# Optimization experiments

Hardware: AMD Instinct MI355X
Metric: run time of the kernel (lower is better)

Reference implementation:

```python
import jax, jax.numpy as jnp
import numpy as np

N_KNN = 16
BN_EPS = 1e-5


def conv1d(x, w, b):
    # x: [B, Cin, N], w: [Cout, Cin], b: [Cout] (1x1 Conv1d)
    return jnp.einsum('oc,bcn->bon', w, x) + b[None, :, None]


def conv2d(x, w, b):
    # x: [B, Cin, N, K], w: [Cout, Cin], b: [Cout] (1x1 Conv2d)
    return jnp.einsum('oc,bcnk->bonk', w, x) + b[None, :, None, None]


def bn2d(x, gamma, beta, mean, var):
    # eval-mode BatchNorm2d over channel axis 1
    scale = (gamma / jnp.sqrt(var + BN_EPS))[None, :, None, None]
    return (x - mean[None, :, None, None]) * scale + beta[None, :, None, None]


def knn_idx(pos, k):
    # pos: [B, 3, N] -> idx: [B, N, K] of k nearest neighbors (incl. self)
    p = jnp.swapaxes(pos, 1, 2)  # [B, N, 3]
    sq = jnp.sum(p * p, axis=-1)  # [B, N]
    d2 = sq[:, :, None] - 2.0 * jnp.einsum('bnd,bmd->bnm', p, p) + sq[:, None, :]
    _, idx = jax.lax.top_k(-d2, k)
    return idx


def group(x, idx):
    # x: [B, C, N], idx: [B, N, K] -> [B, C, N, K] (grouping_operation)
    return jax.vmap(lambda xb, ib: xb[:, ib])(x, idx)


def setup_inputs() -> dict:
    key = jax.random.key(0)
    B, C_OBJ, C_Q, N, DIM, PH, AM = 4, 512, 512, 4096, 128, 64, 4
    ks = jax.random.split(key, 32)
    r = lambda i, sh, s=0.05: jax.random.normal(ks[i], sh, jnp.float32) * s
    inp = {
        'obj_feature': jax.random.normal(ks[0], (B, C_OBJ, N), jnp.float32),
        'pos': jax.random.normal(ks[1], (B, 3, N), jnp.float32),
        'query_points': jax.random.normal(ks[2], (B, C_Q, N), jnp.float32),
        # linear_start_query / linear_start_obj
        'w_sq': r(3, (DIM, C_Q)), 'b_sq': r(4, (DIM,)),
        'w_so': r(5, (DIM, C_OBJ)), 'b_so': r(6, (DIM,)),
        # key / query / value 1x1 convs
        'w_k': r(7, (DIM, DIM)), 'b_k': r(8, (DIM,)),
        'w_q': r(9, (DIM, DIM)), 'b_q': r(10, (DIM,)),
        'w_v': r(11, (DIM, DIM)), 'b_v': r(12, (DIM,)),
        # pos_mlp: Conv2d(3->PH), BN, ReLU, Conv2d(PH->DIM)
        'w_p1': r(13, (PH, 3)), 'b_p1': r(14, (PH,)),
        'g_bn1': 1.0 + r(15, (PH,)), 'be_bn1': r(16, (PH,)),
        'm_bn1': r(17, (PH,)), 'v_bn1': 1.0 + 0.1 * jax.random.uniform(ks[18], (PH,), jnp.float32),
        'w_p2': r(19, (DIM, PH)), 'b_p2': r(20, (DIM,)),
        # attn_mlp: Conv2d(DIM->DIM*AM), BN, ReLU, Conv2d(DIM*AM->DIM)
        'w_a1': r(21, (DIM * AM, DIM)), 'b_a1': r(22, (DIM * AM,)),
        'g_bn2': 1.0 + r(23, (DIM * AM,)), 'be_bn2': r(24, (DIM * AM,)),
        'm_bn2': r(25, (DIM * AM,)), 'v_bn2': 1.0 + 0.1 * jax.random.uniform(ks[26], (DIM * AM,), jnp.float32),
        # linear_end
        'w_e': r(27, (C_OBJ, DIM)), 'b_e': r(28, (C_OBJ,)),
    }
    return inp


def reference(obj_feature, pos, query_points, w_sq, b_sq, w_so, b_so, w_k, b_k,
              w_q, b_q, w_v, b_v, w_p1, b_p1, g_bn1, be_bn1, m_bn1, v_bn1,
              w_p2, b_p2, w_a1, b_a1, g_bn2, be_bn2, m_bn2, v_bn2, w_e, b_e):
    qf = conv1d(query_points, w_sq, b_sq)          # [B, dim, N]
    f = conv1d(obj_feature, w_so, b_so)            # [B, dim, N]
    idx = knn_idx(jax.lax.stop_gradient(pos), N_KNN)  # [B, N, K]
    key_g = group(conv1d(f, w_k, b_k), idx)        # [B, dim, N, K]
    value = conv1d(f, w_v, b_v)                    # [B, dim, N]
    query = conv1d(qf, w_q, b_q)                   # [B, dim, N]
    qk_rel = query[:, :, :, None] - key_g          # [B, dim, N, K]
    pos_rel = pos[:, :, :, None] - group(pos, idx)  # [B, 3, N, K]
    pe = conv2d(jax.nn.relu(bn2d(conv2d(pos_rel, w_p1, b_p1), g_bn1, be_bn1, m_bn1, v_bn1)), w_p2, b_p2)
    attn = conv2d(jax.nn.relu(bn2d(conv2d(qk_rel + pe, w_a1, b_a1), g_bn2, be_bn2, m_bn2, v_bn2)), w_a2_placeholder := w_p2 * 0 + 0, b_p2 * 0) if False else None
    hidden = jax.nn.relu(bn2d(conv2d(qk_rel + pe, w_a1, b_a1), g_bn2, be_bn2, m_bn2, v_bn2))
    attn = jax.nn.softmax(conv2d(hidden, w_a2, b_a2), axis=-1)  # softmax over K
    v = value[:, :, :, None] + pe                  # [B, dim, N, K]
    agg = jnp.sum(attn * v, axis=-1)               # 'b c i j, b c i j -> b c i'
    return conv1d(agg, w_e, b_e)                   # [B, C_obj, N]

# fix: w_a2/b_a2 are parameters; re-declare reference cleanly to include them

def _setup_extra(inp):
    kk = jax.random.split(jax.random.key(7), 2)
    inp['w_a2'] = jax.random.normal(kk[0], (128, 512), jnp.float32) * 0.05
    inp['b_a2'] = jax.random.normal(kk[1], (128,), jnp.float32) * 0.05
    return inp

_orig_setup = setup_inputs

def setup_inputs():
    return _setup_extra(_orig_setup())


def reference(obj_feature, pos, query_points, w_sq, b_sq, w_so, b_so, w_k, b_k,
              w_q, b_q, w_v, b_v, w_p1, b_p1, g_bn1, be_bn1, m_bn1, v_bn1,
              w_p2, b_p2, w_a1, b_a1, g_bn2, be_bn2, m_bn2, v_bn2, w_a2, b_a2,
              w_e, b_e):
    qf = conv1d(query_points, w_sq, b_sq)
    f = conv1d(obj_feature, w_so, b_so)
    idx = knn_idx(jax.lax.stop_gradient(pos), N_KNN)
    key_g = group(conv1d(f, w_k, b_k), idx)
    value = conv1d(f, w_v, b_v)
    query = conv1d(qf, w_q, b_q)
    qk_rel = query[:, :, :, None] - key_g
    pos_rel = pos[:, :, :, None] - group(pos, idx)
    pe = conv2d(jax.nn.relu(bn2d(conv2d(pos_rel, w_p1, b_p1), g_bn1, be_bn1, m_bn1, v_bn1)), w_p2, b_p2)
    hidden = jax.nn.relu(bn2d(conv2d(qk_rel + pe, w_a1, b_a1), g_bn2, be_bn2, m_bn2, v_bn2))
    attn = jax.nn.softmax(conv2d(hidden, w_a2, b_a2), axis=-1)
    v = value[:, :, :, None] + pe
    agg = jnp.sum(attn * v, axis=-1)
    return conv1d(agg, w_e, b_e)
```

## Files before the change

### kernel.cpp

```cpp
#include <hip/hip_runtime.h>

typedef __bf16 bf16;
typedef __bf16 bf16x8 __attribute__((ext_vector_type(8)));
typedef __bf16 bf16x4 __attribute__((ext_vector_type(4)));
typedef __bf16 bf16x2 __attribute__((ext_vector_type(2)));
typedef float f32x4 __attribute__((ext_vector_type(4)));

#define MFMA16(a,b,c) __builtin_amdgcn_mfma_f32_16x16x32_bf16((a),(b),(c),0,0,0)

#define NPTS 4096
#define CIN 512
#define DIM 128
#define PH 64
#define HID 512

#define OFF_WQS 0u
#define OFF_WKO (128u*1024u)
#define OFF_WVO (256u*1024u)
#define OFF_BQS (384u*1024u)
#define OFF_BKO (385u*1024u)
#define OFF_BVO (386u*1024u)
#define OFF_S1  (387u*1024u)
#define OFF_T1  (388u*1024u)
#define OFF_S2  (389u*1024u)
#define OFF_T2  (391u*1024u)
#define OFF_CW  (400u*1024u)
#define OFF_QT  (1u<<20)
#define OFF_KT  (OFF_QT + (4u<<20))
#define OFF_VT  (OFF_QT + (8u<<20))
#define OFF_IDX (OFF_QT + (12u<<20))
#define WS_NEED (OFF_QT + (13u<<20))

struct P {
  const float* in[31];
  char* ws;
  float* out;
};

__global__ __launch_bounds__(256) void k_fold(P p) {
  int tid = blockIdx.x*256 + threadIdx.x;
  char* ws = p.ws;
  if (tid < 196608) {
    int m_id = tid >> 16, o = (tid >> 9) & 127, c = tid & 511;
    const float* A  = m_id==0 ? p.in[9] : (m_id==1 ? p.in[7] : p.in[11]);
    const float* Bm = (m_id==0) ? p.in[3] : p.in[5];
    float acc = 0.f;
    #pragma unroll 8
    for (int m=0;m<128;m++) acc += A[o*128+m] * Bm[m*512+c];
    bf16* outw = (bf16*)(ws + (m_id==0?OFF_WQS: m_id==1?OFF_WKO:OFF_WVO));
    outw[o*512+c] = (bf16)acc;
  } else if (tid < 196992) {
    int t = tid - 196608; int m_id = t >> 7, o = t & 127;
    const float* A  = m_id==0 ? p.in[9] : (m_id==1 ? p.in[7] : p.in[11]);
    const float* bb = (m_id==0) ? p.in[4] : p.in[6];
    const float* bs = m_id==0 ? p.in[10] : (m_id==1 ? p.in[8] : p.in[12]);
    float acc = bs[o];
    for (int m=0;m<128;m++) acc += A[o*128+m] * bb[m];
    float* ob = (float*)(ws + (m_id==0?OFF_BQS: m_id==1?OFF_BKO:OFF_BVO));
    ob[o] = acc;
  } else if (tid < 197056) {
    int i = tid - 196992;
    float s = p.in[15][i] * rsqrtf(p.in[18][i] + 1e-5f);
    ((float*)(ws+OFF_S1))[i] = s;
    ((float*)(ws+OFF_T1))[i] = (p.in[14][i] - p.in[17][i])*s + p.in[16][i];
  } else if (tid < 197568) {
    int i = tid - 197056;
    float s = p.in[23][i] * rsqrtf(p.in[26][i] + 1e-5f);
    ((float*)(ws+OFF_S2))[i] = s;
    ((float*)(ws+OFF_T2))[i] = (p.in[22][i] - p.in[25][i])*s + p.in[24][i];
  } else if (tid < 223168) {
    int e0 = (tid - 197568) * 8;
    const float* src; int base;
    if (e0 < 8192)        { src = p.in[19]; base = 0; }
    else if (e0 < 73728)  { src = p.in[21]; base = 8192; }
    else if (e0 < 139264) { src = p.in[29]; base = 73728; }
    else                  { src = p.in[27]; base = 139264; }
    const float* sp = src + (e0 - base);
    f32x4 a = *(const f32x4*)sp, b2 = *(const f32x4*)(sp+4);
    bf16x8 o8;
    o8[0]=(bf16)a[0]; o8[1]=(bf16)a[1]; o8[2]=(bf16)a[2]; o8[3]=(bf16)a[3];
    o8[4]=(bf16)b2[0]; o8[5]=(bf16)b2[1]; o8[6]=(bf16)b2[2]; o8[7]=(bf16)b2[3];
    *(bf16x8*)((bf16*)(ws+OFF_CW) + e0) = o8;
  }
}

__global__ __launch_bounds__(256) void k_knn(P p) {
  int lane = threadIdx.x & 63, w = threadIdx.x >> 6;
  int ig = blockIdx.x*4 + w;
  int b = ig >> 12, n = ig & 4095;
  const float* pb = p.in[1] + b*3*NPTS;
  float qx = pb[n], qy = pb[NPTS+n], qz = pb[2*NPTS+n];
  float sqn = __fadd_rn(__fadd_rn(__fmul_rn(qx,qx), __fmul_rn(qy,qy)), __fmul_rn(qz,qz));
  float d2a[64];
  #pragma unroll
  for (int t=0;t<64;t++) {
    int j = t*64 + lane;
    float xj=pb[j], yj=pb[NPTS+j], zj=pb[2*NPTS+j];
    float sqj = __fadd_rn(__fadd_rn(__fmul_rn(xj,xj), __fmul_rn(yj,yj)), __fmul_rn(zj,zj));
    float dot = __fadd_rn(__fadd_rn(__fmul_rn(qx,xj), __fmul_rn(qy,yj)), __fmul_rn(qz,zj));
    d2a[t] = __fadd_rn(__fsub_rn(sqn, __fmul_rn(2.f,dot)), sqj);
  }
  int* op = (int*)(p.ws + OFF_IDX) + ig*16;
  long long prev = -1ll;
  for (int r=0;r<16;r++) {
    long long best = 0x7fffffffffffffffll;
    #pragma unroll
    for (int t=0;t<64;t++) {
      long long key = ((long long)(int)__float_as_uint(d2a[t]) << 32) | (long long)(t*64+lane);
      if (key > prev && key < best) best = key;
    }
    #pragma unroll
    for (int off=32; off>0; off>>=1) {
      long long o = __shfl_xor(best, off);
      best = best < o ? best : o;
    }
    prev = best;
    if (lane==0) op[r] = (int)best & 4095;
  }
}

__global__ __launch_bounds__(256) void k_qkv(P p) {
  int mat = blockIdx.z, b = blockIdx.y, n0 = blockIdx.x*64;
  int tid = threadIdx.x, lane = tid&63, w = tid>>6;
  const float* in = (mat==0 ? p.in[2] : p.in[0]) + b*CIN*NPTS;
  const bf16* W = (const bf16*)(p.ws + (mat==0?OFF_WQS: mat==1?OFF_WKO:OFF_WVO));
  const float* bias = (const float*)(p.ws + (mat==0?OFF_BQS: mat==1?OFF_BKO:OFF_BVO));
  bf16* outT = (bf16*)(p.ws + (mat==0?OFF_QT: mat==1?OFF_KT:OFF_VT)) + (b*NPTS + n0)*DIM;
  __shared__ __align__(16) bf16 Bl[64*40];
  f32x4 acc[8] = {};
  for (int ks=0; ks<16; ks++) {
    int c0 = ks*32;
    {
      int cc = tid>>3, nn0 = (tid&7)*8;
      const float* sp = in + (c0+cc)*NPTS + n0 + nn0;
      f32x4 a = *(const f32x4*)sp, b2 = *(const f32x4*)(sp+4);
      Bl[(nn0+0)*40+cc]=(bf16)a[0];  Bl[(nn0+1)*40+cc]=(bf16)a[1];
      Bl[(nn0+2)*40+cc]=(bf16)a[2];  Bl[(nn0+3)*40+cc]=(bf16)a[3];
      Bl[(nn0+4)*40+cc]=(bf16)b2[0]; Bl[(nn0+5)*40+cc]=(bf16)b2[1];
      Bl[(nn0+6)*40+cc]=(bf16)b2[2]; Bl[(nn0+7)*40+cc]=(bf16)b2[3];
    }
    __syncthreads();
    int ncol = w*16 + (lane&15);
    bf16x8 bfr = *(const bf16x8*)(&Bl[ncol*40 + (lane>>4)*8]);
    #pragma unroll
    for (int ot=0;ot<8;ot++) {
      bf16x8 af = *(const bf16x8*)(W + (ot*16 + (lane&15))*CIN + c0 + (lane>>4)*8);
      acc[ot] = MFMA16(af, bfr, acc[ot]);
    }
    __syncthreads();
  }
  int o0 = (lane>>4)*4;
  int nloc = w*16 + (lane&15);
  #pragma unroll
  for (int ot=0;ot<8;ot++) {
    f32x4 bs = *(const f32x4*)(bias + ot*16 + o0);
    bf16x4 st;
    st[0]=(bf16)(acc[ot][0]+bs[0]); st[1]=(bf16)(acc[ot][1]+bs[1]);
    st[2]=(bf16)(acc[ot][2]+bs[2]); st[3]=(bf16)(acc[ot][3]+bs[3]);
    *(bf16x4*)(outT + nloc*DIM + ot*16 + o0) = st;
  }
}

__global__ __launch_bounds__(512) void k_fused(P p) {
  int b = blockIdx.y, pt0 = blockIdx.x*8;
  int tid=threadIdx.x, lane=tid&63, w=tid>>6;
  char* ws = p.ws;
  const bf16* qT = (const bf16*)(ws+OFF_QT) + b*NPTS*DIM;
  const bf16* kT = (const bf16*)(ws+OFF_KT) + b*NPTS*DIM;
  const bf16* vT = (const bf16*)(ws+OFF_VT) + b*NPTS*DIM;
  const int* idxg = (const int*)(ws+OFF_IDX) + (b*NPTS + pt0)*16;
  const bf16* wp2b = (const bf16*)(ws+OFF_CW);
  const bf16* wa1b = wp2b + 8192;
  const bf16* wa2b = wa1b + 65536;
  const bf16* web  = wa2b + 65536;
  __shared__ __align__(16) bf16 Xl[128*136];
  __shared__ __align__(16) bf16 HT[128*72];
  __shared__ __align__(16) bf16 aggl[16*136];
  __shared__ float prl[128][4];
  __shared__ int idxl[128];

  if (tid < 128) {
    int pt = tid>>4;
    int j = idxg[tid] & 4095;
    idxl[tid] = j;
    const float* pb = p.in[1] + b*3*NPTS;
    int n = pt0+pt;
    prl[tid][0] = pb[n]        - pb[j];
    prl[tid][1] = pb[NPTS+n]   - pb[NPTS+j];
    prl[tid][2] = pb[2*NPTS+n] - pb[2*NPTS+j];
  } else if (tid >= 256 && tid < 392) {
    f32x4 z = {};
    *(f32x4*)((char*)aggl + 2176 + (tid-256)*16) = z;
  }
  __syncthreads();

  {
    int col = tid & 127, mb = (tid>>7)*16;
    float r0=prl[col][0], r1=prl[col][1], r2=prl[col][2];
    const float* wp1 = p.in[13];
    const float* s1 = (const float*)(ws+OFF_S1);
    const float* t1 = (const float*)(ws+OFF_T1);
    #pragma unroll
    for (int i=0;i<16;i+=2) {
      int m = mb+i;
      float x0 = wp1[m*3]*r0   + wp1[m*3+1]*r1 + wp1[m*3+2]*r2;
      float x1 = wp1[m*3+3]*r0 + wp1[m*3+4]*r1 + wp1[m*3+5]*r2;
      bf16x2 pk;
      pk[0] = (bf16)fmaxf(0.f, x0*s1[m]   + t1[m]);
      pk[1] = (bf16)fmaxf(0.f, x1*s1[m+1] + t1[m+1]);
      *(bf16x2*)(&HT[col*72 + m]) = pk;
    }
  }
  __syncthreads();

  {
    f32x4 acc[8] = {};
    int crow = w*16 + (lane&15);
    #pragma unroll
    for (int ksx=0; ksx<2; ksx++) {
      int m0 = ksx*32 + (lane>>4)*8;
      bf16x8 af = *(const bf16x8*)(wp2b + crow*PH + m0);
      #pragma unroll
      for (int nt=0; nt<8; nt++) {
        int col = nt*16 + (lane&15);
        bf16x8 bfr = *(const bf16x8*)(&HT[col*72 + m0]);
        acc[nt] = MFMA16(af, bfr, acc[nt]);
      }
    }
    int c0 = w*16 + (lane>>4)*4;
    f32x4 bp4 = *(const f32x4*)(p.in[20] + c0);
    #pragma unroll
    for (int nt=0; nt<8; nt++) {
      int col = nt*16 + (lane&15);
      int j = idxl[col];
      int n = pt0 + nt;
      bf16x4 q4 = *(const bf16x4*)(qT + n*DIM + c0);
      bf16x4 k4 = *(const bf16x4*)(kT + j*DIM + c0);
      bf16x4 st;
      #pragma unroll
      for (int r=0;r<4;r++)
        st[r] = (bf16)((float)q4[r] - (float)k4[r] + acc[nt][r] + bp4[r]);
      *(bf16x4*)(&Xl[col*136 + c0]) = st;
    }
  }
  __syncthreads();

  f32x4 S[8] = {};
  const float* s2 = (const float*)(ws+OFF_S2);
  const float* t2 = (const float*)(ws+OFF_T2);
  for (int ch=0; ch<8; ch++) {
    f32x4 acc1[4] = {};
    int mtw = w & 3, nbase = (w>>2)*4;
    int hrow = ch*64 + mtw*16 + (lane&15);
    #pragma unroll
    for (int ksx=0; ksx<4; ksx++) {
      bf16x8 af = *(const bf16x8*)(wa1b + hrow*DIM + ksx*32 + (lane>>4)*8);
      #pragma unroll
      for (int i=0; i<4; i++) {
        int col = (nbase+i)*16 + (lane&15);
        bf16x8 bfr = *(const bf16x8*)(&Xl[col*136 + ksx*32 + (lane>>4)*8]);
        acc1[i] = MFMA16(af, bfr, acc1[i]);
      }
    }
    int h0 = ch*64 + mtw*16 + (lane>>4)*4;
    int h0loc = mtw*16 + (lane>>4)*4;
    f32x4 sv = *(const f32x4*)(s2 + h0);
    f32x4 tv = *(const f32x4*)(t2 + h0);
    #pragma unroll
    for (int i=0;i<4;i++) {
      int col = (nbase+i)*16 + (lane&15);
      bf16x4 st;
      st[0]=(bf16)fmaxf(0.f, acc1[i][0]*sv[0]+tv[0]);
      st[1]=(bf16)fmaxf(0.f, acc1[i][1]*sv[1]+tv[1]);
      st[2]=(bf16)fmaxf(0.f, acc1[i][2]*sv[2]+tv[2]);
      st[3]=(bf16)fmaxf(0.f, acc1[i][3]*sv[3]+tv[3]);
      *(bf16x4*)(&HT[col*72 + h0loc]) = st;
    }
    __syncthreads();
    int orow = w*16 + (lane&15);
    #pragma unroll
    for (int ksx=0; ksx<2; ksx++) {
      bf16x8 af = *(const bf16x8*)(wa2b + orow*HID + ch*64 + ksx*32 + (lane>>4)*8);
      #pragma unroll
      for (int nt=0; nt<8; nt++) {
        int col = nt*16 + (lane&15);
        bf16x8 bfr = *(const bf16x8*)(&HT[col*72 + ksx*32 + (lane>>4)*8]);
        S[nt] = MFMA16(af, bfr, S[nt]);
      }
    }
    __syncthreads();
  }

  {
    int c0 = w*16 + (lane>>4)*4;
    #pragma unroll
    for (int nt=0; nt<8; nt++) {
      f32x4 s = S[nt];
      float at[4];
      #pragma unroll
      for (int r=0;r<4;r++) {
        float mx = s[r];
        #pragma unroll
        for (int mk=8; mk; mk>>=1) mx = fmaxf(mx, __shfl_xor(mx, mk));
        float e = __expf(s[r]-mx);
        float sum = e;
        #pragma unroll
        for (int mk=8; mk; mk>>=1) sum += __shfl_xor(sum, mk);
        at[r] = e / sum;
      }
      int col = nt*16 + (lane&15);
      int j = idxl[col];
      int n = pt0 + nt;
      bf16x4 x4 = *(const bf16x4*)(&Xl[col*136 + c0]);
      bf16x4 q4 = *(const bf16x4*)(qT + n*DIM + c0);
      bf16x4 k4 = *(const bf16x4*)(kT + j*DIM + c0);
      bf16x4 v4 = *(const bf16x4*)(vT + n*DIM + c0);
      float ag[4];
      #pragma unroll
      for (int r=0;r<4;r++) {
        float vpe = (float)v4[r] + (float)x4[r] - (float)q4[r] + (float)k4[r];
        float cab = at[r]*vpe;
        #pragma unroll
        for (int mk=8; mk; mk>>=1) cab += __shfl_xor(cab, mk);
        ag[r] = cab;
      }
      if ((lane&15)==0) {
        bf16x4 st;
        st[0]=(bf16)ag[0]; st[1]=(bf16)ag[1]; st[2]=(bf16)ag[2]; st[3]=(bf16)ag[3];
        *(bf16x4*)(&aggl[nt*136 + c0]) = st;
      }
    }
  }
  __syncthreads();

  {
    const float* be = p.in[28];
    f32x4 acc5[4] = {};
    #pragma unroll
    for (int ksx=0; ksx<4; ksx++) {
      int pcol = lane&15;
      bf16x8 bfr = *(const bf16x8*)(&aggl[pcol*136 + ksx*32 + (lane>>4)*8]);
      #pragma unroll
      for (int i=0;i<4;i++) {
        int e = (w*4+i)*16 + (lane&15);
        bf16x8 af = *(const bf16x8*)(web + e*DIM + ksx*32 + (lane>>4)*8);
        acc5[i] = MFMA16(af, bfr, acc5[i]);
      }
    }
    int ptc = lane&15;
    if (ptc < 8) {
      int n = pt0 + ptc;
      #pragma unroll
      for (int i=0;i<4;i++) {
        int e0 = (w*4+i)*16 + (lane>>4)*4;
        f32x4 be4 = *(const f32x4*)(be + e0);
        #pragma unroll
        for (int r=0;r<4;r++)
          p.out[(b*CIN + e0+r)*NPTS + n] = acc5[i][r] + be4[r];
      }
    }
  }
}

extern "C" void kernel_launch(void* const* d_in, const int* in_sizes, int n_in,
                              void* d_out, int out_size, void* d_ws, size_t ws_size,
                              hipStream_t stream) {
  if (ws_size < WS_NEED || n_in < 31) return;
  P p;
  for (int i=0;i<31;i++) p.in[i] = (const float*)d_in[i];
  p.ws = (char*)d_ws;
  p.out = (float*)d_out;
  k_fold<<<872, 256, 0, stream>>>(p);
  k_knn<<<4096, 256, 0, stream>>>(p);
  k_qkv<<<dim3(64, 4, 3), 256, 0, stream>>>(p);
  k_fused<<<dim3(512, 4), 512, 0, stream>>>(p);
}
```

Measured before the change: 457.3 us.

## Give each wave one point and keep attention MLP activations in registers

The fused attention kernel is restructured so that each wave handles one query point with its 16 neighbours. Intermediate activations (position encoding, qk+pe input, hidden layer) stay in registers and are redistributed between MFMA layouts with cross-lane shuffles, which removes the shared-memory round trips and per-chunk block barriers. The softmax and aggregation reductions now use DPP row rotations instead of shfl_xor, and the kNN kernel precomputes its 64-bit sort keys once rather than rebuilding them on each of the 16 selection passes. In exchange, each wave now streams all of the attention MLP weights from global/L2 by itself with no sharing across waves, and register pressure rises, including 64 long-long keys per thread in kNN.

```diff
diff --git a/kernel.cpp b/kernel.cpp
--- a/kernel.cpp
+++ b/kernel.cpp
@@ -24,6 +24,7 @@
 #define OFF_T1  (388u*1024u)
 #define OFF_S2  (389u*1024u)
 #define OFF_T2  (391u*1024u)
+#define OFF_W1P (394u*1024u)
 #define OFF_CW  (400u*1024u)
 #define OFF_QT  (1u<<20)
 #define OFF_KT  (OFF_QT + (4u<<20))
@@ -36,6 +37,29 @@
   char* ws;
   float* out;
 };
+
+__device__ __forceinline__ unsigned pack2(float a, float b){
+  union { bf16x2 h; unsigned u; } z; z.h[0]=(bf16)a; z.h[1]=(bf16)b; return z.u;
+}
+template<int C> __device__ __forceinline__ float rorf(float x){
+  return __int_as_float(__builtin_amdgcn_mov_dpp(__float_as_int(x), 0x120|C, 0xF, 0xF, true));
+}
+__device__ __forceinline__ float red16max(float x){
+  x=fmaxf(x,rorf<1>(x)); x=fmaxf(x,rorf<2>(x)); x=fmaxf(x,rorf<4>(x)); x=fmaxf(x,rorf<8>(x)); return x;
+}
+__device__ __forceinline__ float red16sum(float x){
+  x+=rorf<1>(x); x+=rorf<2>(x); x+=rorf<4>(x); x+=rorf<8>(x); return x;
+}
+__device__ __forceinline__ bf16x8 redist(unsigned pa0, unsigned pa1, unsigned pb0, unsigned pb1,
+                                         int src0, int src1, bool selhi){
+  union { unsigned u[4]; bf16x8 v; } z;
+  unsigned a0=(unsigned)__shfl((int)pa0,src0), a1=(unsigned)__shfl((int)pa1,src0);
+  unsigned a2=(unsigned)__shfl((int)pa0,src1), a3=(unsigned)__shfl((int)pa1,src1);
+  unsigned b0=(unsigned)__shfl((int)pb0,src0), b1=(unsigned)__shfl((int)pb1,src0);
+  unsigned b2=(unsigned)__shfl((int)pb0,src1), b3=(unsigned)__shfl((int)pb1,src1);
+  z.u[0]=selhi?b0:a0; z.u[1]=selhi?b1:a1; z.u[2]=selhi?b2:a2; z.u[3]=selhi?b3:a3;
+  return z.v;
+}
 
 __global__ __launch_bounds__(256) void k_fold(P p) {
   int tid = blockIdx.x*256 + threadIdx.x;
@@ -81,6 +105,12 @@
     o8[0]=(bf16)a[0]; o8[1]=(bf16)a[1]; o8[2]=(bf16)a[2]; o8[3]=(bf16)a[3];
     o8[4]=(bf16)b2[0]; o8[5]=(bf16)b2[1]; o8[6]=(bf16)b2[2]; o8[7]=(bf16)b2[3];
     *(bf16x8*)((bf16*)(ws+OFF_CW) + e0) = o8;
+  } else if (tid < 223232) {
+    int m = tid - 223168;
+    const float* wp1 = p.in[13];
+    float s = p.in[15][m] * rsqrtf(p.in[18][m] + 1e-5f);
+    f32x4 v; v[0]=wp1[3*m]; v[1]=wp1[3*m+1]; v[2]=wp1[3*m+2]; v[3]=s;
+    *(f32x4*)((char*)(ws+OFF_W1P) + m*16) = v;
   }
 }
 
@@ -91,14 +121,15 @@
   const float* pb = p.in[1] + b*3*NPTS;
   float qx = pb[n], qy = pb[NPTS+n], qz = pb[2*NPTS+n];
   float sqn = __fadd_rn(__fadd_rn(__fmul_rn(qx,qx), __fmul_rn(qy,qy)), __fmul_rn(qz,qz));
-  float d2a[64];
+  long long keys[64];
   #pragma unroll
   for (int t=0;t<64;t++) {
     int j = t*64 + lane;
     float xj=pb[j], yj=pb[NPTS+j], zj=pb[2*NPTS+j];
     float sqj = __fadd_rn(__fadd_rn(__fmul_rn(xj,xj), __fmul_rn(yj,yj)), __fmul_rn(zj,zj));
     float dot = __fadd_rn(__fadd_rn(__fmul_rn(qx,xj), __fmul_rn(qy,yj)), __fmul_rn(qz,zj));
-    d2a[t] = __fadd_rn(__fsub_rn(sqn, __fmul_rn(2.f,dot)), sqj);
+    float d2 = __fadd_rn(__fsub_rn(sqn, __fmul_rn(2.f,dot)), sqj);
+    keys[t] = ((long long)(int)__float_as_uint(d2) << 32) | (long long)j;
   }
   int* op = (int*)(p.ws + OFF_IDX) + ig*16;
   long long prev = -1ll;
@@ -106,8 +137,8 @@
     long long best = 0x7fffffffffffffffll;
     #pragma unroll
     for (int t=0;t<64;t++) {
-      long long key = ((long long)(int)__float_as_uint(d2a[t]) << 32) | (long long)(t*64+lane);
-      if (key > prev && key < best) best = key;
+      long long k2 = keys[t];
+      if (k2 > prev && k2 < best) best = k2;
     }
     #pragma unroll
     for (int off=32; off>0; off>>=1) {
@@ -162,177 +193,125 @@
 }
 
 __global__ __launch_bounds__(512) void k_fused(P p) {
-  int b = blockIdx.y, pt0 = blockIdx.x*8;
+  int bb = blockIdx.y, pt0 = blockIdx.x*8;
   int tid=threadIdx.x, lane=tid&63, w=tid>>6;
+  int c = lane&15, g = lane>>4;
   char* ws = p.ws;
-  const bf16* qT = (const bf16*)(ws+OFF_QT) + b*NPTS*DIM;
-  const bf16* kT = (const bf16*)(ws+OFF_KT) + b*NPTS*DIM;
-  const bf16* vT = (const bf16*)(ws+OFF_VT) + b*NPTS*DIM;
-  const int* idxg = (const int*)(ws+OFF_IDX) + (b*NPTS + pt0)*16;
+  const bf16* qT = (const bf16*)(ws+OFF_QT) + bb*NPTS*DIM;
+  const bf16* kT = (const bf16*)(ws+OFF_KT) + bb*NPTS*DIM;
+  const bf16* vT = (const bf16*)(ws+OFF_VT) + bb*NPTS*DIM;
   const bf16* wp2b = (const bf16*)(ws+OFF_CW);
   const bf16* wa1b = wp2b + 8192;
   const bf16* wa2b = wa1b + 65536;
   const bf16* web  = wa2b + 65536;
-  __shared__ __align__(16) bf16 Xl[128*136];
-  __shared__ __align__(16) bf16 HT[128*72];
-  __shared__ __align__(16) bf16 aggl[16*136];
-  __shared__ float prl[128][4];
-  __shared__ int idxl[128];
-
-  if (tid < 128) {
-    int pt = tid>>4;
-    int j = idxg[tid] & 4095;
-    idxl[tid] = j;
-    const float* pb = p.in[1] + b*3*NPTS;
-    int n = pt0+pt;
-    prl[tid][0] = pb[n]        - pb[j];
-    prl[tid][1] = pb[NPTS+n]   - pb[NPTS+j];
-    prl[tid][2] = pb[2*NPTS+n] - pb[2*NPTS+j];
-  } else if (tid >= 256 && tid < 392) {
-    f32x4 z = {};
-    *(f32x4*)((char*)aggl + 2176 + (tid-256)*16) = z;
-  }
-  __syncthreads();
-
-  {
-    int col = tid & 127, mb = (tid>>7)*16;
-    float r0=prl[col][0], r1=prl[col][1], r2=prl[col][2];
-    const float* wp1 = p.in[13];
-    const float* s1 = (const float*)(ws+OFF_S1);
-    const float* t1 = (const float*)(ws+OFF_T1);
-    #pragma unroll
-    for (int i=0;i<16;i+=2) {
-      int m = mb+i;
-      float x0 = wp1[m*3]*r0   + wp1[m*3+1]*r1 + wp1[m*3+2]*r2;
-      float x1 = wp1[m*3+3]*r0 + wp1[m*3+4]*r1 + wp1[m*3+5]*r2;
-      bf16x2 pk;
-      pk[0] = (bf16)fmaxf(0.f, x0*s1[m]   + t1[m]);
-      pk[1] = (bf16)fmaxf(0.f, x1*s1[m+1] + t1[m+1]);
-      *(bf16x2*)(&HT[col*72 + m]) = pk;
-    }
-  }
-  __syncthreads();
-
-  {
-    f32x4 acc[8] = {};
-    int crow = w*16 + (lane&15);
-    #pragma unroll
-    for (int ksx=0; ksx<2; ksx++) {
-      int m0 = ksx*32 + (lane>>4)*8;
-      bf16x8 af = *(const bf16x8*)(wp2b + crow*PH + m0);
-      #pragma unroll
-      for (int nt=0; nt<8; nt++) {
-        int col = nt*16 + (lane&15);
-        bf16x8 bfr = *(const bf16x8*)(&HT[col*72 + m0]);
-        acc[nt] = MFMA16(af, bfr, acc[nt]);
-      }
-    }
-    int c0 = w*16 + (lane>>4)*4;
-    f32x4 bp4 = *(const f32x4*)(p.in[20] + c0);
-    #pragma unroll
-    for (int nt=0; nt<8; nt++) {
-      int col = nt*16 + (lane&15);
-      int j = idxl[col];
-      int n = pt0 + nt;
-      bf16x4 q4 = *(const bf16x4*)(qT + n*DIM + c0);
-      bf16x4 k4 = *(const bf16x4*)(kT + j*DIM + c0);
-      bf16x4 st;
-      #pragma unroll
-      for (int r=0;r<4;r++)
-        st[r] = (bf16)((float)q4[r] - (float)k4[r] + acc[nt][r] + bp4[r]);
-      *(bf16x4*)(&Xl[col*136 + c0]) = st;
-    }
-  }
-  __syncthreads();
-
-  f32x4 S[8] = {};
   const float* s2 = (const float*)(ws+OFF_S2);
   const float* t2 = (const float*)(ws+OFF_T2);
-  for (int ch=0; ch<8; ch++) {
-    f32x4 acc1[4] = {};
-    int mtw = w & 3, nbase = (w>>2)*4;
-    int hrow = ch*64 + mtw*16 + (lane&15);
-    #pragma unroll
-    for (int ksx=0; ksx<4; ksx++) {
-      bf16x8 af = *(const bf16x8*)(wa1b + hrow*DIM + ksx*32 + (lane>>4)*8);
+  __shared__ __align__(16) bf16 aggl[16*136];
+
+  if (tid < 136) { f32x4 z = {}; *(f32x4*)((char*)aggl + 2176 + tid*16) = z; }
+
+  int pt = pt0 + w;
+  int jc = ((const int*)(ws+OFF_IDX))[(bb*NPTS + pt)*16 + c];
+  const float* pb = p.in[1] + bb*3*NPTS;
+  float pr0 = pb[pt]-pb[jc], pr1 = pb[NPTS+pt]-pb[NPTS+jc], pr2 = pb[2*NPTS+pt]-pb[2*NPTS+jc];
+
+  const f32x4* wt4 = (const f32x4*)(ws+OFF_W1P);
+  const float* t1t = (const float*)(ws+OFF_T1);
+  bf16x8 tb[2];
+  #pragma unroll
+  for (int ks=0;ks<2;ks++){
+    #pragma unroll
+    for (int jj=0;jj<8;jj++){
+      int m = ks*32 + g*8 + jj;
+      f32x4 wv = wt4[m];
+      float x = wv[0]*pr0 + wv[1]*pr1 + wv[2]*pr2;
+      tb[ks][jj] = (bf16)fmaxf(0.f, x*wv[3] + t1t[m]);
+    }
+  }
+  f32x4 pef[8] = {};
+  #pragma unroll
+  for (int mt=0;mt<8;mt++){
+    #pragma unroll
+    for (int ks=0;ks<2;ks++){
+      bf16x8 af = *(const bf16x8*)(wp2b + (mt*16+c)*PH + ks*32 + g*8);
+      pef[mt] = MFMA16(af, tb[ks], pef[mt]);
+    }
+  }
+  unsigned pk[8][2];
+  const float* bp2 = p.in[20];
+  #pragma unroll
+  for (int mt=0;mt<8;mt++){
+    f32x4 bp = *(const f32x4*)(bp2 + mt*16 + g*4);
+    pk[mt][0] = pack2(pef[mt][0]+bp[0], pef[mt][1]+bp[1]);
+    pk[mt][1] = pack2(pef[mt][2]+bp[2], pef[mt][3]+bp[3]);
+  }
+  int src0 = c + ((lane&16)<<1);
+  int src1 = src0 + 16;
+  bool selhi = (g>=2);
+  bf16x8 xf[4];
+  #pragma unroll
+  for (int ksx=0;ksx<4;ksx++){
+    bf16x8 pe8 = redist(pk[2*ksx][0],pk[2*ksx][1],pk[2*ksx+1][0],pk[2*ksx+1][1],src0,src1,selhi);
+    bf16x8 q8 = *(const bf16x8*)(qT + pt*DIM + ksx*32 + g*8);
+    bf16x8 k8 = *(const bf16x8*)(kT + jc*DIM + ksx*32 + g*8);
+    #pragma unroll
+    for (int jj=0;jj<8;jj++)
+      xf[ksx][jj] = (bf16)((float)q8[jj] - (float)k8[jj] + (float)pe8[jj]);
+  }
+  f32x4 S[8] = {};
+  #pragma unroll 1
+  for (int ch=0;ch<8;ch++){
+    f32x4 acc[4] = {};
+    #pragma unroll
+    for (int ksx=0;ksx<4;ksx++){
       #pragma unroll
-      for (int i=0; i<4; i++) {
-        int col = (nbase+i)*16 + (lane&15);
-        bf16x8 bfr = *(const bf16x8*)(&Xl[col*136 + ksx*32 + (lane>>4)*8]);
-        acc1[i] = MFMA16(af, bfr, acc1[i]);
+      for (int mt2=0;mt2<4;mt2++){
+        bf16x8 af = *(const bf16x8*)(wa1b + (ch*64+mt2*16+c)*DIM + ksx*32 + g*8);
+        acc[mt2] = MFMA16(af, xf[ksx], acc[mt2]);
       }
     }
-    int h0 = ch*64 + mtw*16 + (lane>>4)*4;
-    int h0loc = mtw*16 + (lane>>4)*4;
-    f32x4 sv = *(const f32x4*)(s2 + h0);
-    f32x4 tv = *(const f32x4*)(t2 + h0);
-    #pragma unroll
-    for (int i=0;i<4;i++) {
-      int col = (nbase+i)*16 + (lane&15);
-      bf16x4 st;
-      st[0]=(bf16)fmaxf(0.f, acc1[i][0]*sv[0]+tv[0]);
-      st[1]=(bf16)fmaxf(0.f, acc1[i][1]*sv[1]+tv[1]);
-      st[2]=(bf16)fmaxf(0.f, acc1[i][2]*sv[2]+tv[2]);
-      st[3]=(bf16)fmaxf(0.f, acc1[i][3]*sv[3]+tv[3]);
-      *(bf16x4*)(&HT[col*72 + h0loc]) = st;
-    }
-    __syncthreads();
-    int orow = w*16 + (lane&15);
-    #pragma unroll
-    for (int ksx=0; ksx<2; ksx++) {
-      bf16x8 af = *(const bf16x8*)(wa2b + orow*HID + ch*64 + ksx*32 + (lane>>4)*8);
-      #pragma unroll
-      for (int nt=0; nt<8; nt++) {
-        int col = nt*16 + (lane&15);
-        bf16x8 bfr = *(const bf16x8*)(&HT[col*72 + ksx*32 + (lane>>4)*8]);
-        S[nt] = MFMA16(af, bfr, S[nt]);
-      }
-    }
-    __syncthreads();
-  }
-
-  {
-    int c0 = w*16 + (lane>>4)*4;
-    #pragma unroll
-    for (int nt=0; nt<8; nt++) {
-      f32x4 s = S[nt];
-      float at[4];
-      #pragma unroll
-      for (int r=0;r<4;r++) {
-        float mx = s[r];
-        #pragma unroll
-        for (int mk=8; mk; mk>>=1) mx = fmaxf(mx, __shfl_xor(mx, mk));
-        float e = __expf(s[r]-mx);
-        float sum = e;
-        #pragma unroll
-        for (int mk=8; mk; mk>>=1) sum += __shfl_xor(sum, mk);
-        at[r] = e / sum;
-      }
-      int col = nt*16 + (lane&15);
-      int j = idxl[col];
-      int n = pt0 + nt;
-      bf16x4 x4 = *(const bf16x4*)(&Xl[col*136 + c0]);
-      bf16x4 q4 = *(const bf16x4*)(qT + n*DIM + c0);
-      bf16x4 k4 = *(const bf16x4*)(kT + j*DIM + c0);
-      bf16x4 v4 = *(const bf16x4*)(vT + n*DIM + c0);
-      float ag[4];
-      #pragma unroll
-      for (int r=0;r<4;r++) {
-        float vpe = (float)v4[r] + (float)x4[r] - (float)q4[r] + (float)k4[r];
-        float cab = at[r]*vpe;
-        #pragma unroll
-        for (int mk=8; mk; mk>>=1) cab += __shfl_xor(cab, mk);
-        ag[r] = cab;
-      }
-      if ((lane&15)==0) {
-        bf16x4 st;
-        st[0]=(bf16)ag[0]; st[1]=(bf16)ag[1]; st[2]=(bf16)ag[2]; st[3]=(bf16)ag[3];
-        *(bf16x4*)(&aggl[nt*136 + c0]) = st;
-      }
+    unsigned pk2[4][2];
+    #pragma unroll
+    for (int mt2=0;mt2<4;mt2++){
+      int h0 = ch*64 + mt2*16 + g*4;
+      f32x4 sv = *(const f32x4*)(s2 + h0);
+      f32x4 tv = *(const f32x4*)(t2 + h0);
+      float r0 = fmaxf(0.f, acc[mt2][0]*sv[0]+tv[0]);
+      float r1 = fmaxf(0.f, acc[mt2][1]*sv[1]+tv[1]);
+      float r2 = fmaxf(0.f, acc[mt2][2]*sv[2]+tv[2]);
+      float r3 = fmaxf(0.f, acc[mt2][3]*sv[3]+tv[3]);
+      pk2[mt2][0] = pack2(r0,r1); pk2[mt2][1] = pack2(r2,r3);
+    }
+    bf16x8 hf0 = redist(pk2[0][0],pk2[0][1],pk2[1][0],pk2[1][1],src0,src1,selhi);
+    bf16x8 hf1 = redist(pk2[2][0],pk2[2][1],pk2[3][0],pk2[3][1],src0,src1,selhi);
+    #pragma unroll
+    for (int ot=0;ot<8;ot++){
+      bf16x8 af0 = *(const bf16x8*)(wa2b + (ot*16+c)*HID + ch*64 + g*8);
+      S[ot] = MFMA16(af0, hf0, S[ot]);
+      bf16x8 af1 = *(const bf16x8*)(wa2b + (ot*16+c)*HID + ch*64 + 32 + g*8);
+      S[ot] = MFMA16(af1, hf1, S[ot]);
+    }
+  }
+  #pragma unroll
+  for (int ot=0;ot<8;ot++){
+    bf16x4 v4 = *(const bf16x4*)(vT + pt*DIM + ot*16 + g*4);
+    union { unsigned u[2]; bf16x4 h; } pc; pc.u[0]=pk[ot][0]; pc.u[1]=pk[ot][1];
+    float agv[4];
+    #pragma unroll
+    for (int r=0;r<4;r++){
+      float mx = red16max(S[ot][r]);
+      float e = __expf(S[ot][r]-mx);
+      float sm = red16sum(e);
+      float at = e/sm;
+      float vpe = (float)v4[r] + (float)pc.h[r];
+      agv[r] = red16sum(at*vpe);
+    }
+    if (c==0){
+      bf16x4 st; st[0]=(bf16)agv[0]; st[1]=(bf16)agv[1]; st[2]=(bf16)agv[2]; st[3]=(bf16)agv[3];
+      *(bf16x4*)(&aggl[w*136 + ot*16 + g*4]) = st;
     }
   }
   __syncthreads();
-
   {
     const float* be = p.in[28];
     f32x4 acc5[4] = {};
@@ -356,7 +335,7 @@
         f32x4 be4 = *(const f32x4*)(be + e0);
         #pragma unroll
         for (int r=0;r<4;r++)
-          p.out[(b*CIN + e0+r)*NPTS + n] = acc5[i][r] + be4[r];
+          p.out[(bb*CIN + e0+r)*NPTS + n] = acc5[i][r] + be4[r];
       }
     }
   }
```

Result: slower. 810.1 us (+77.2%).
